# Kernel optimization log

Measured on AMD Instinct MI355X. Metric: run time of the kernel, lower is better.

The kernel has to match this reference:

```python
import jax, jax.numpy as jnp
import numpy as np
from jax import lax

PORTION = 0.1
IOU_TH = 0.25
C = 20  # VOC classes


def greedy_nms(iou_sub, thr):
    """Greedy NMS over candidates already sorted by descending score.
    iou_sub: (K,K) IoU map restricted to candidates. Returns (K,) bool keep mask.
    Matches instance_nms: pop highest score, drop all with iou >= thr."""
    K = iou_sub.shape[0]

    def body(i, state):
        alive, keep = state
        sel = alive[i]
        keep = keep.at[i].set(sel)
        suppress = iou_sub[i] >= thr
        alive = jnp.where(sel, alive & ~suppress, alive)
        return (alive, keep)

    alive0 = jnp.ones((K,), dtype=bool)
    keep0 = jnp.zeros((K,), dtype=bool)
    _, keep = lax.fori_loop(0, K, body, (alive0, keep0))
    return keep


def setup_inputs() -> dict:
    N = 6144
    key = jax.random.key(0)
    k1, k2, k3, k4, k5 = jax.random.split(key, 5)
    predict_cls = jax.random.uniform(k1, (N, C + 1), dtype=jnp.float32)
    predict_det = jax.random.uniform(k2, (N, C + 1), dtype=jnp.float32)
    rois = jax.random.uniform(k3, (N, 5), dtype=jnp.float32) * 512.0
    labels = jax.random.randint(k4, (C,), 0, 2, dtype=jnp.int32)
    labels = labels.at[0].set(1)  # guarantee at least one positive class
    u = jax.random.uniform(k5, (N, N), dtype=jnp.float32)
    iou_map = 0.5 * (u + u.T)  # symmetric, like a precomputed mask-IoU map
    iou_map = iou_map.at[jnp.arange(N), jnp.arange(N)].set(1.0)
    return {"predict_cls": predict_cls, "predict_det": predict_det,
            "rois": rois, "labels": labels, "iou_map": iou_map}


def reference(predict_cls, predict_det, rois, labels, iou_map):
    # forward(..., diffuse=False) -> mist_label path
    rois = rois[:, 1:]                      # strip batch-index column
    preds = predict_cls * predict_det       # (N, C+1)
    preds = preds[:, 1:]                    # drop background col -> (N, C)
    N = preds.shape[0]
    K = int(np.ceil(PORTION * N))           # keep_count

    gt_labels = jnp.zeros((N, C + 1), dtype=preds.dtype)
    gt_weights = -jnp.ones((N,), dtype=preds.dtype)

    # sequential per-class updates (order matters for gt_weights comparisons)
    for c in range(C):
        cls_prob = preds[:, c]
        order = jnp.argsort(-cls_prob)[:K]                       # top-K by score, descending
        sub = iou_map[order[:, None], order[None, :]]            # (K,K)
        keep = greedy_nms(sub, IOU_TH)                           # (K,) bool
        nms_mask = jnp.zeros((N,), dtype=bool).at[order].set(keep)
        upd = nms_mask & (cls_prob > gt_weights) & (labels[c] > 0)
        onehot = jax.nn.one_hot(c + 1, C + 1, dtype=preds.dtype)
        gt_labels = jnp.where(upd[:, None], onehot, gt_labels)
        gt_weights = jnp.where(upd, cls_prob, gt_weights)

    gt_idxs = jnp.sum(gt_labels, axis=-1) > 0                    # (N,) gt mask
    # overlaps = iou_map[:, gt_idxs], kept full-width with non-gt cols masked to -1
    overlaps = jnp.where(gt_idxs[None, :], iou_map, -1.0)
    max_v = jnp.max(overlaps, axis=-1)
    max_i = jnp.argmax(overlaps, axis=-1)

    pseudo_labels = gt_labels[max_i]                             # (N, C+1)
    loss_weights = gt_weights[max_i]                             # (N,)
    pseudo_iou_label = max_v

    ignore = max_v == 0
    pseudo_labels = jnp.where(ignore[:, None], 0.0, pseudo_labels)
    loss_weights = jnp.where(ignore, 0.0, loss_weights)
    bg = (max_v < IOU_TH) & ~ignore
    bg_onehot = jax.nn.one_hot(0, C + 1, dtype=preds.dtype)
    pseudo_labels = jnp.where(bg[:, None], bg_onehot, pseudo_labels)

    return pseudo_labels, pseudo_iou_label, loss_weights
```

## Files before the change

### kernel.cpp

```cpp
#include <hip/hip_runtime.h>
#include <stdint.h>

#define N_ROIS 6144
#define NCLS 20
#define NC1 21
#define TOPK 615
#define IOU_TH 0.25f
#define BUCKETS 8192
#define CAND 1024
#define KEEP_CAP 128
#define EMAX 640

__global__ __launch_bounds__(256) void k_prep(const float* __restrict__ pc,
                                              const float* __restrict__ pd,
                                              float* __restrict__ preds_t) {
  __shared__ float tile[256 * NC1];
  const int tid = threadIdx.x;
  const int base = blockIdx.x * 256;
  const size_t g = (size_t)base * NC1;
  for (int i = tid; i < 256 * NC1; i += 256) tile[i] = pc[g + i] * pd[g + i];
  __syncthreads();
  #pragma unroll
  for (int c = 0; c < NCLS; ++c)
    preds_t[(size_t)c * N_ROIS + base + tid] = tile[tid * NC1 + (c + 1)];
}

__global__ __launch_bounds__(512) void k_select_nms(
    const float* __restrict__ preds_t, const int* __restrict__ labels,
    const float* __restrict__ iou,
    int* __restrict__ kept_cnt, int2* __restrict__ kept_pairs) {
  const int c = blockIdx.x;
  if (labels[c] <= 0) return;
  __shared__ int hist[BUCKETS];
  __shared__ unsigned long long key[CAND];
  __shared__ int chunk[512];
  __shared__ int wsum[8];
  __shared__ unsigned long long wmin[8];
  __shared__ int s_tb, s_need, s_cnt;
  const int tid = threadIdx.x;
  const int lane = tid & 63, wid = tid >> 6;

  for (int i = tid; i < BUCKETS; i += 512) hist[i] = 0;
  for (int i = tid; i < CAND; i += 512) key[i] = ~0ull;
  if (tid == 0) s_cnt = 0;
  __syncthreads();

  float sc[12];
  #pragma unroll
  for (int k = 0; k < 12; ++k) {
    int n = tid + (k << 9);
    float s = preds_t[(size_t)c * N_ROIS + n];
    sc[k] = s;
    int b = (int)(s * (float)BUCKETS);
    b = min(max(b, 0), BUCKETS - 1);
    atomicAdd(&hist[b], 1);
  }
  __syncthreads();

  int own = 0;
  #pragma unroll
  for (int k = 0; k < 16; ++k) own += hist[BUCKETS - 1 - (tid * 16 + k)];
  chunk[tid] = own;
  int r = own;
  #pragma unroll
  for (int m = 1; m < 64; m <<= 1) r += __shfl_xor(r, m, 64);
  if (lane == 0) wsum[wid] = r;
  __syncthreads();

  if (tid == 0) {
    int cum = 0, w = 0;
    for (; w < 7; ++w) { if (cum + wsum[w] >= TOPK) break; cum += wsum[w]; }
    int t = w << 6;
    for (;; ++t) { if (cum + chunk[t] >= TOPK) break; cum += chunk[t]; }
    int tb = 0, need = TOPK - cum;
    #pragma unroll
    for (int k = 0; k < 16; ++k) {
      int b = BUCKETS - 1 - (t * 16 + k);
      int h = hist[b];
      if (cum + h >= TOPK) { tb = b; need = TOPK - cum; break; }
      cum += h;
    }
    s_tb = tb; s_need = need;
  }
  __syncthreads();
  const int tb = s_tb, need = s_need;

  #pragma unroll
  for (int k = 0; k < 12; ++k) {
    float s = sc[k];
    int b = (int)(s * (float)BUCKETS);
    b = min(max(b, 0), BUCKETS - 1);
    if (b >= tb) {
      int pos = atomicAdd(&s_cnt, 1);
      if (pos < CAND) {
        unsigned bits = __float_as_uint(s);
        key[pos] = ((unsigned long long)(~bits) << 32) | (unsigned)(tid + (k << 9));
      }
    }
  }
  __syncthreads();

  const int cnt = min(s_cnt, CAND);
  for (int sl = tid; sl < CAND; sl += 512) {
    unsigned long long mykey = key[sl];
    bool demote = false;
    if (sl < cnt && mykey != ~0ull) {
      unsigned bits = ~(unsigned)(mykey >> 32);
      float s = __uint_as_float(bits);
      int b = (int)(s * (float)BUCKETS);
      b = min(max(b, 0), BUCKETS - 1);
      if (b == tb) {
        int rank = 0;
        for (int j = 0; j < cnt; ++j) {
          unsigned long long kj = key[j];
          if (kj < mykey) {
            unsigned bj = ~(unsigned)(kj >> 32);
            float sj = __uint_as_float(bj);
            int bb = (int)(sj * (float)BUCKETS);
            bb = min(max(bb, 0), BUCKETS - 1);
            if (bb == tb) ++rank;
          }
        }
        demote = (rank >= need);
      }
    }
    __syncthreads();
    if (demote) key[sl] = ~0ull;
    __syncthreads();
  }

  int npop = 0;
  while (true) {
    unsigned long long v = key[tid];
    { unsigned long long v2 = key[tid + 512]; if (v2 < v) v = v2; }
    #pragma unroll
    for (int m = 1; m < 64; m <<= 1) {
      unsigned lo = __shfl_xor((unsigned)v, m, 64);
      unsigned hi = __shfl_xor((unsigned)(v >> 32), m, 64);
      unsigned long long u = ((unsigned long long)hi << 32) | lo;
      if (u < v) v = u;
    }
    if (lane == 0) wmin[wid] = v;
    __syncthreads();
    unsigned long long win = wmin[0];
    #pragma unroll
    for (int w = 1; w < 8; ++w) if (wmin[w] < win) win = wmin[w];
    if (win == ~0ull) break;
    const int bi = (int)(win & 0xffffffffu);
    const float* row = iou + (size_t)bi * N_ROIS;
    for (int sl = tid; sl < CAND; sl += 512) {
      unsigned long long kk = key[sl];
      if (kk == ~0ull) continue;
      if (kk == win && npop < KEEP_CAP)
        kept_pairs[c * KEEP_CAP + npop] = make_int2(bi, (int)(~(unsigned)(win >> 32)));
      int n = (int)(kk & 0xffffffffu);
      if (row[n] >= IOU_TH) key[sl] = ~0ull;
    }
    ++npop;
    __syncthreads();
  }
  if (tid == 0) kept_cnt[c] = min(npop, KEEP_CAP);
}

__global__ __launch_bounds__(256) void k_out(
    const float* __restrict__ iou, const int* __restrict__ labels,
    const int* __restrict__ kept_cnt, const int2* __restrict__ kept_pairs,
    float* __restrict__ out) {
  __shared__ int   e_n[EMAX];
  __shared__ float e_s[EMAX];
  __shared__ short e_c[EMAX];
  __shared__ unsigned char e_ok[EMAX];
  __shared__ int s_E;
  const int tid = threadIdx.x;
  if (tid == 0) s_E = 0;
  __syncthreads();
  if (tid < NCLS && labels[tid] > 0) {
    int cnt = min(kept_cnt[tid], KEEP_CAP);
    for (int t = 0; t < cnt; ++t) {
      int2 pr = kept_pairs[tid * KEEP_CAP + t];
      int p = atomicAdd(&s_E, 1);
      if (p < EMAX) { e_n[p] = pr.x; e_s[p] = __int_as_float(pr.y); e_c[p] = (short)tid; }
    }
  }
  __syncthreads();
  const int E = min(s_E, EMAX);
  for (int i = tid; i < E; i += 256) {
    int n = e_n[i]; float s = e_s[i]; int cc = e_c[i];
    bool ok = true;
    for (int j = 0; j < E; ++j) {
      if (j == i || e_n[j] != n) continue;
      float sj = e_s[j];
      if (sj > s || (sj == s && e_c[j] < cc)) { ok = false; break; }
    }
    e_ok[i] = ok ? 1 : 0;
  }
  __syncthreads();

  const int n = blockIdx.x * 256 + tid;
  float maxv = -1.0f;
  int mslot = -1, mn = N_ROIS;
  for (int j = 0; j < E; ++j) {
    if (!e_ok[j]) continue;
    int nj = e_n[j];
    float v = iou[(size_t)nj * N_ROIS + n];
    if (v > maxv || (v == maxv && nj < mn)) { maxv = v; mn = nj; mslot = j; }
  }
  float lw; int pl;
  if (mslot >= 0) { lw = e_s[mslot]; pl = (int)e_c[mslot] + 1; }
  else { lw = -1.0f; pl = 0; }
  bool ignore = (maxv == 0.0f);
  bool bg = (maxv < IOU_TH) && !ignore;
  float row[NC1];
  #pragma unroll
  for (int k = 0; k < NC1; ++k) row[k] = 0.0f;
  if (ignore) lw = 0.0f;
  else if (bg) row[0] = 1.0f;
  else row[pl] = 1.0f;
  #pragma unroll
  for (int k = 0; k < NC1; ++k) out[(size_t)n * NC1 + k] = row[k];
  out[(size_t)N_ROIS * NC1 + n] = maxv;
  out[(size_t)N_ROIS * NC1 + N_ROIS + n] = lw;
}

extern "C" void kernel_launch(void* const* d_in, const int* in_sizes, int n_in,
                              void* d_out, int out_size, void* d_ws, size_t ws_size,
                              hipStream_t stream) {
  const float* pc     = (const float*)d_in[0];
  const float* pd     = (const float*)d_in[1];
  const int*   labels = (const int*)d_in[3];
  const float* iou    = (const float*)d_in[4];
  float* out = (float*)d_out;

  char* ws = (char*)d_ws;
  float* preds_t  = (float*)ws;
  int2*  kept_pairs = (int2*)(ws + (size_t)NCLS * N_ROIS * 4);
  int*   kept_cnt = (int*)((char*)kept_pairs + NCLS * KEEP_CAP * 8);

  k_prep      <<<N_ROIS / 256, 256, 0, stream>>>(pc, pd, preds_t);
  k_select_nms<<<NCLS, 512, 0, stream>>>(preds_t, labels, iou, kept_cnt, kept_pairs);
  k_out       <<<N_ROIS / 256, 256, 0, stream>>>(iou, labels, kept_cnt, kept_pairs, out);
}
```

Before: 275.6 us.

## Build deduplicated GT table once in separate kernel and parallelize top-K threshold scan

Moves the per-block gathering and deduplication of kept NMS entries out of k_out into a single-block k_table kernel. That kernel writes a compacted table of live GT entries, so each of the 24 k_out blocks no longer repeats the O(E^2) dedup and its loop skips dead entries. The top-K bucket search now uses a parallel prefix scan instead of a serial thread-0 walk, and the table gather uses 8 threads per class. The cost is one extra kernel launch and a dependency on packing the ROI index and class into 16-bit fields.

New measurement: 274.2 us. About the same (-0.5%).

```diff
diff --git a/kernel.cpp b/kernel.cpp
--- a/kernel.cpp
+++ b/kernel.cpp
@@ -33,7 +33,6 @@
   if (labels[c] <= 0) return;
   __shared__ int hist[BUCKETS];
   __shared__ unsigned long long key[CAND];
-  __shared__ int chunk[512];
   __shared__ int wsum[8];
   __shared__ unsigned long long wmin[8];
   __shared__ int s_tb, s_need, s_cnt;
@@ -41,7 +40,7 @@
   const int lane = tid & 63, wid = tid >> 6;
 
   for (int i = tid; i < BUCKETS; i += 512) hist[i] = 0;
-  for (int i = tid; i < CAND; i += 512) key[i] = ~0ull;
+  key[tid] = ~0ull; key[tid + 512] = ~0ull;
   if (tid == 0) s_cnt = 0;
   __syncthreads();
 
@@ -60,22 +59,22 @@
   int own = 0;
   #pragma unroll
   for (int k = 0; k < 16; ++k) own += hist[BUCKETS - 1 - (tid * 16 + k)];
-  chunk[tid] = own;
-  int r = own;
-  #pragma unroll
-  for (int m = 1; m < 64; m <<= 1) r += __shfl_xor(r, m, 64);
-  if (lane == 0) wsum[wid] = r;
-  __syncthreads();
-
-  if (tid == 0) {
-    int cum = 0, w = 0;
-    for (; w < 7; ++w) { if (cum + wsum[w] >= TOPK) break; cum += wsum[w]; }
-    int t = w << 6;
-    for (;; ++t) { if (cum + chunk[t] >= TOPK) break; cum += chunk[t]; }
-    int tb = 0, need = TOPK - cum;
+  int inc = own;
+  #pragma unroll
+  for (int m = 1; m < 64; m <<= 1) {
+    int v = __shfl_up(inc, m, 64);
+    if (lane >= m) inc += v;
+  }
+  if (lane == 63) wsum[wid] = inc;
+  __syncthreads();
+  #pragma unroll
+  for (int w = 0; w < 8; ++w) inc += (w < wid) ? wsum[w] : 0;
+  int exc = inc - own;
+  if (exc < TOPK && inc >= TOPK) {
+    int cum = exc, tb = 0, need = TOPK - cum;
     #pragma unroll
     for (int k = 0; k < 16; ++k) {
-      int b = BUCKETS - 1 - (t * 16 + k);
+      int b = BUCKETS - 1 - (tid * 16 + k);
       int h = hist[b];
       if (cum + h >= TOPK) { tb = b; need = TOPK - cum; break; }
       cum += h;
@@ -162,24 +161,27 @@
   if (tid == 0) kept_cnt[c] = min(npop, KEEP_CAP);
 }
 
-__global__ __launch_bounds__(256) void k_out(
-    const float* __restrict__ iou, const int* __restrict__ labels,
-    const int* __restrict__ kept_cnt, const int2* __restrict__ kept_pairs,
-    float* __restrict__ out) {
+__global__ __launch_bounds__(256) void k_table(
+    const int* __restrict__ labels, const int* __restrict__ kept_cnt,
+    const int2* __restrict__ kept_pairs,
+    int2* __restrict__ gt_tab, int* __restrict__ gt_cnt) {
   __shared__ int   e_n[EMAX];
   __shared__ float e_s[EMAX];
   __shared__ short e_c[EMAX];
-  __shared__ unsigned char e_ok[EMAX];
-  __shared__ int s_E;
-  const int tid = threadIdx.x;
-  if (tid == 0) s_E = 0;
-  __syncthreads();
-  if (tid < NCLS && labels[tid] > 0) {
-    int cnt = min(kept_cnt[tid], KEEP_CAP);
-    for (int t = 0; t < cnt; ++t) {
-      int2 pr = kept_pairs[tid * KEEP_CAP + t];
-      int p = atomicAdd(&s_E, 1);
-      if (p < EMAX) { e_n[p] = pr.x; e_s[p] = __int_as_float(pr.y); e_c[p] = (short)tid; }
+  __shared__ int2  dense[EMAX];
+  __shared__ int s_E, s_live;
+  const int tid = threadIdx.x;
+  if (tid == 0) { s_E = 0; s_live = 0; }
+  __syncthreads();
+  if (tid < NCLS * 8) {
+    int c = tid >> 3;
+    if (labels[c] > 0) {
+      int cnt = min(kept_cnt[c], KEEP_CAP);
+      for (int i = tid & 7; i < cnt; i += 8) {
+        int2 pr = kept_pairs[c * KEEP_CAP + i];
+        int p = atomicAdd(&s_E, 1);
+        if (p < EMAX) { e_n[p] = pr.x; e_s[p] = __int_as_float(pr.y); e_c[p] = (short)c; }
+      }
     }
   }
   __syncthreads();
@@ -192,21 +194,42 @@
       float sj = e_s[j];
       if (sj > s || (sj == s && e_c[j] < cc)) { ok = false; break; }
     }
-    e_ok[i] = ok ? 1 : 0;
+    if (ok) {
+      int p = atomicAdd(&s_live, 1);
+      dense[p] = make_int2(n | (cc << 16), __float_as_int(s));
+    }
+  }
+  __syncthreads();
+  const int L = min(s_live, EMAX);
+  for (int i = tid; i < L; i += 256) gt_tab[i] = dense[i];
+  if (tid == 0) *gt_cnt = L;
+}
+
+__global__ __launch_bounds__(256) void k_out(
+    const float* __restrict__ iou, const int2* __restrict__ gt_tab,
+    const int* __restrict__ gt_cnt, float* __restrict__ out) {
+  __shared__ int   e_nj[EMAX];
+  __shared__ int   e_cls[EMAX];
+  __shared__ float e_sc[EMAX];
+  const int tid = threadIdx.x;
+  const int E = *gt_cnt;
+  for (int i = tid; i < E; i += 256) {
+    int2 v = gt_tab[i];
+    e_nj[i] = v.x & 0xFFFF; e_cls[i] = v.x >> 16; e_sc[i] = __int_as_float(v.y);
   }
   __syncthreads();
 
   const int n = blockIdx.x * 256 + tid;
   float maxv = -1.0f;
   int mslot = -1, mn = N_ROIS;
+  #pragma unroll 4
   for (int j = 0; j < E; ++j) {
-    if (!e_ok[j]) continue;
-    int nj = e_n[j];
+    int nj = e_nj[j];
     float v = iou[(size_t)nj * N_ROIS + n];
     if (v > maxv || (v == maxv && nj < mn)) { maxv = v; mn = nj; mslot = j; }
   }
   float lw; int pl;
-  if (mslot >= 0) { lw = e_s[mslot]; pl = (int)e_c[mslot] + 1; }
+  if (mslot >= 0) { lw = e_sc[mslot]; pl = e_cls[mslot] + 1; }
   else { lw = -1.0f; pl = 0; }
   bool ignore = (maxv == 0.0f);
   bool bg = (maxv < IOU_TH) && !ignore;
@@ -232,11 +255,15 @@
   float* out = (float*)d_out;
 
   char* ws = (char*)d_ws;
-  float* preds_t  = (float*)ws;
-  int2*  kept_pairs = (int2*)(ws + (size_t)NCLS * N_ROIS * 4);
-  int*   kept_cnt = (int*)((char*)kept_pairs + NCLS * KEEP_CAP * 8);
+  size_t off = 0;
+  float* preds_t    = (float*)(ws + off); off += (size_t)NCLS * N_ROIS * 4;
+  int2*  kept_pairs = (int2*)(ws + off);  off += (size_t)NCLS * KEEP_CAP * 8;
+  int*   kept_cnt   = (int*)(ws + off);   off += 128;
+  int2*  gt_tab     = (int2*)(ws + off);  off += (size_t)EMAX * 8;
+  int*   gt_cnt     = (int*)(ws + off);   off += 4;
 
   k_prep      <<<N_ROIS / 256, 256, 0, stream>>>(pc, pd, preds_t);
   k_select_nms<<<NCLS, 512, 0, stream>>>(preds_t, labels, iou, kept_cnt, kept_pairs);
-  k_out       <<<N_ROIS / 256, 256, 0, stream>>>(iou, labels, kept_cnt, kept_pairs, out);
-}
+  k_table     <<<1, 256, 0, stream>>>(labels, kept_cnt, kept_pairs, gt_tab, gt_cnt);
+  k_out       <<<N_ROIS / 256, 256, 0, stream>>>(iou, gt_tab, gt_cnt, out);
+}
```
